# Performance work log

Hardware: AMD Instinct MI355X
Metric: run time of the kernel (lower is better)

The kernel has to match this reference:

```python
import jax, jax.numpy as jnp
import numpy as np

NEG = -1e32
EPS_LN = 1e-5

def _layer_norm(x, w, b):
    mu = jnp.mean(x, axis=-1, keepdims=True)
    var = jnp.mean((x - mu) ** 2, axis=-1, keepdims=True)
    return (x - mu) / jnp.sqrt(var + EPS_LN) * w + b

def setup_inputs() -> dict:
    key = jax.random.key(0)
    ks = jax.random.split(key, 10)
    B, S, D, H, F = 2, 2048, 1024, 16, 4096
    s = 0.02
    return {
        "query": jax.random.normal(ks[0], (B, S, D), jnp.float32),
        "key": jax.random.normal(ks[1], (B, S, D), jnp.float32),
        "values": jax.random.normal(ks[2], (B, S, D), jnp.float32),
        "Wk": jax.random.normal(ks[3], (D, D), jnp.float32) * s,
        "bk": jnp.zeros((D,), jnp.float32),
        "Wv": jax.random.normal(ks[4], (D, D), jnp.float32) * s,
        "bv": jnp.zeros((D,), jnp.float32),
        "Wo": jax.random.normal(ks[5], (D, D), jnp.float32) * s,
        "bo": jnp.zeros((D,), jnp.float32),
        "gammas": jax.random.normal(ks[6], (H, 1, 1), jnp.float32),
        "ln1_w": jnp.ones((D,), jnp.float32),
        "ln1_b": jnp.zeros((D,), jnp.float32),
        "W1": jax.random.normal(ks[7], (F, D), jnp.float32) * s,
        "b1": jnp.zeros((F,), jnp.float32),
        "W2": jax.random.normal(ks[8], (D, F), jnp.float32) * s,
        "b2": jnp.zeros((D,), jnp.float32),
        "ln2_w": jnp.ones((D,), jnp.float32),
        "ln2_b": jnp.zeros((D,), jnp.float32),
        "mask": 1,
    }

def _forward(query, key, values, Wk, bk, Wv, bv, Wo, bo, gammas,
             ln1_w, ln1_b, W1, b1, W2, b2, ln2_w, ln2_b, mask):
    B, S, D = query.shape
    H = gammas.shape[0]
    dk = D // H
    # kq_same=True: q and k both use k_linear
    def proj(x, W, b):
        return (x @ W.T + b).reshape(B, S, H, dk).transpose(0, 2, 1, 3)  # bhsd
    q = proj(query, Wk, bk)
    k = proj(key, Wk, bk)
    v = proj(values, Wv, bv)

    scores = jnp.einsum("bhqd,bhkd->bhqk", q, k) / np.sqrt(dk).astype(np.float32)
    # src_mask: np.triu(ones, k=mask)==0 -> allowed where j <= i + mask - 1
    allow = jnp.tril(jnp.ones((S, S), bool), k=mask - 1)[None, None]  # (1,1,S,S)

    # --- distance decay (no_grad block in torch) ---
    scores_ = jax.nn.softmax(jnp.where(allow, scores, NEG), axis=-1)
    scores_ = scores_ * allow.astype(scores_.dtype)
    distcum = jnp.cumsum(scores_, axis=-1)
    disttotal = jnp.sum(scores_, axis=-1, keepdims=True)
    idx = jnp.arange(S)
    position_effect = jnp.abs(idx[:, None] - idx[None, :]).astype(jnp.float32)[None, None]
    dist_scores = jnp.sqrt(jnp.clip((disttotal - distcum) * position_effect, 0.0, None))
    gamma = -jax.nn.softplus(gammas)[None]  # (1,H,1,1)
    total_effect = jnp.clip(jnp.exp(dist_scores * gamma), 1e-5, 1e5)
    total_effect = jax.lax.stop_gradient(total_effect)
    # ---

    scores = scores * total_effect
    scores = jnp.where(allow, scores, NEG)
    attn = jax.nn.softmax(scores, axis=-1)
    out = jnp.einsum("bhqk,bhkd->bhqd", attn, v)
    concat = out.transpose(0, 2, 1, 3).reshape(B, S, D)
    query2 = concat @ Wo.T + bo

    x = _layer_norm(query + query2, ln1_w, ln1_b)
    ff = jax.nn.relu(x @ W1.T + b1) @ W2.T + b2
    x = _layer_norm(x + ff, ln2_w, ln2_b)
    return x

def reference(query, key, values, Wk, bk, Wv, bv, Wo, bo, gammas,
              ln1_w, ln1_b, W1, b1, W2, b2, ln2_w, ln2_b, mask):
    return _forward(query, key, values, Wk, bk, Wv, bv, Wo, bo, gammas,
                    ln1_w, ln1_b, W1, b1, W2, b2, ln2_w, ln2_b, mask)
```

## Files before the change

### kernel.cpp

```cpp
#include <hip/hip_runtime.h>
#include <hip/hip_bf16.h>

#define B_   2
#define S_   2048
#define D_   1024
#define H_   16
#define DK_  64
#define F_   4096
#define M_   (B_*S_)
#define PD   72

typedef __attribute__((ext_vector_type(8))) short short8;
typedef __attribute__((ext_vector_type(4))) float f32x4;

__device__ __forceinline__ float bf2f(unsigned short s) { return __uint_as_float(((unsigned int)s) << 16); }
__device__ __forceinline__ unsigned short f2bf(float f) {
    unsigned int u = __float_as_uint(f);
    u += 0x7fffu + ((u >> 16) & 1u);
    return (unsigned short)(u >> 16);
}

__device__ __forceinline__ bool probe_f32(const unsigned int* p) {
    return *p == 0x3F800000u;
}
__device__ __forceinline__ float ld1e(const void* p, size_t idx, bool f32) {
    return f32 ? ((const float*)p)[idx] : bf2f(((const unsigned short*)p)[idx]);
}
__device__ __forceinline__ void st1e(void* p, size_t idx, bool f32, float v) {
    if (f32) ((float*)p)[idx] = v;
    else     ((unsigned short*)p)[idx] = f2bf(v);
}

__device__ __forceinline__ void async16(void* lds, const void* g) {
    __builtin_amdgcn_global_load_lds(
        (const __attribute__((address_space(1))) void*)g,
        (__attribute__((address_space(3))) void*)lds, 16, 0, 0);
}

__device__ __forceinline__ unsigned int cvt_pk_bf16(float a, float b) {
    unsigned int r;
    asm("v_cvt_pk_bf16_f32 %0, %1, %2" : "=v"(r) : "v"(a), "v"(b));
    return r;
}

template <bool IS_MAX>
__device__ __forceinline__ float block_reduce(float val, float* buf, int tid) {
    buf[tid] = val;
    __syncthreads();
    #pragma unroll
    for (int off = 128; off > 0; off >>= 1) {
        if (tid < off) {
            float o = buf[tid + off];
            buf[tid] = IS_MAX ? fmaxf(buf[tid], o) : (buf[tid] + o);
        }
        __syncthreads();
    }
    float r = buf[0];
    __syncthreads();
    return r;
}

__global__ __launch_bounds__(256) void cvt_all(
    const void* __restrict__ W1, const void* __restrict__ W2,
    const void* __restrict__ Wk, const void* __restrict__ Wv,
    const void* __restrict__ Wo,
    const void* __restrict__ Qi, const void* __restrict__ Ki,
    const void* __restrict__ Vi,
    unsigned short* __restrict__ W1b, unsigned short* __restrict__ W2b,
    unsigned short* __restrict__ Wkb, unsigned short* __restrict__ Wvb,
    unsigned short* __restrict__ Wob,
    unsigned short* __restrict__ qcb, unsigned short* __restrict__ kcb,
    unsigned short* __restrict__ vcb,
    const unsigned int* __restrict__ probe)
{
    const bool p32 = probe_f32(probe);
    const int blk = blockIdx.x;
    const void* src;
    unsigned short* dst;
    int off;
    if (blk < 2048)      { src = W1; dst = W1b; off = blk; }
    else if (blk < 4096) { src = W2; dst = W2b; off = blk - 2048; }
    else if (blk < 4608) { src = Wk; dst = Wkb; off = blk - 4096; }
    else if (blk < 5120) { src = Wv; dst = Wvb; off = blk - 4608; }
    else if (blk < 5632) { src = Wo; dst = Wob; off = blk - 5120; }
    else if (blk < 7680) { if (!p32) return; src = Qi; dst = qcb; off = blk - 5632; }
    else if (blk < 9728) { if (!p32) return; src = Ki; dst = kcb; off = blk - 7680; }
    else                 { if (!p32) return; src = Vi; dst = vcb; off = blk - 9728; }
    const int i8 = (off * 256 + threadIdx.x) * 8;
    if (p32) {
        const float4 a = *(const float4*)((const float*)src + i8);
        const float4 b = *(const float4*)((const float*)src + i8 + 4);
        short8 o;
        o[0] = (short)f2bf(a.x); o[1] = (short)f2bf(a.y);
        o[2] = (short)f2bf(a.z); o[3] = (short)f2bf(a.w);
        o[4] = (short)f2bf(b.x); o[5] = (short)f2bf(b.y);
        o[6] = (short)f2bf(b.z); o[7] = (short)f2bf(b.w);
        *(short8*)(dst + i8) = o;
    } else {
        *(uint4*)(dst + i8) = *(const uint4*)((const unsigned short*)src + i8);
    }
}

template <int RELU, int AEXT, int CEXT>
__device__ __forceinline__ void gemm_body(
    const void* __restrict__ A,
    const unsigned short* __restrict__ W,
    const void* __restrict__ bias,
    void* __restrict__ C,
    int M, int N, int K, bool p32, int bx, int by)
{
    __shared__ unsigned short As[2][128 * 32];
    __shared__ unsigned short Ws[2][128 * 32];

    const bool a32 = AEXT && p32;
    const bool c32 = CEXT && p32;

    const int tid = threadIdx.x;
    const int lane = tid & 63;
    const int w = tid >> 6;
    const int wr = w >> 1;
    const int wc = w & 1;
    const int col16 = lane & 15;
    const int quad = lane >> 4;

    const int m0 = by * 128;
    const int n0 = bx * 128;

    const int c0 = tid, c1 = 256 + tid;
    const int r0 = c0 >> 2, kc0 = (c0 & 3) * 8;
    const int r1 = c1 >> 2, kc1 = (c1 & 3) * 8;

    f32x4 acc[4][4];
    #pragma unroll
    for (int mt = 0; mt < 4; mt++)
        #pragma unroll
        for (int nt = 0; nt < 4; nt++)
            acc[mt][nt] = (f32x4){0.f, 0.f, 0.f, 0.f};

    auto stage = [&](int bb, int k0) {
        async16(&Ws[bb][c0 * 8], W + (size_t)(n0 + r0) * K + k0 + kc0);
        async16(&Ws[bb][c1 * 8], W + (size_t)(n0 + r1) * K + k0 + kc1);
        if (a32) {
            const float* a0 = (const float*)A + (size_t)(m0 + r0) * K + k0 + kc0;
            const float* a1 = (const float*)A + (size_t)(m0 + r1) * K + k0 + kc1;
            const float4 x0 = *(const float4*)a0, y0 = *(const float4*)(a0 + 4);
            const float4 x1 = *(const float4*)a1, y1 = *(const float4*)(a1 + 4);
            short8 s0, s1;
            s0[0] = (short)f2bf(x0.x); s0[1] = (short)f2bf(x0.y);
            s0[2] = (short)f2bf(x0.z); s0[3] = (short)f2bf(x0.w);
            s0[4] = (short)f2bf(y0.x); s0[5] = (short)f2bf(y0.y);
            s0[6] = (short)f2bf(y0.z); s0[7] = (short)f2bf(y0.w);
            s1[0] = (short)f2bf(x1.x); s1[1] = (short)f2bf(x1.y);
            s1[2] = (short)f2bf(x1.z); s1[3] = (short)f2bf(x1.w);
            s1[4] = (short)f2bf(y1.x); s1[5] = (short)f2bf(y1.y);
            s1[6] = (short)f2bf(y1.z); s1[7] = (short)f2bf(y1.w);
            *(short8*)&As[bb][c0 * 8] = s0;
            *(short8*)&As[bb][c1 * 8] = s1;
        } else {
            const unsigned short* Ab = (const unsigned short*)A;
            async16(&As[bb][c0 * 8], Ab + (size_t)(m0 + r0) * K + k0 + kc0);
            async16(&As[bb][c1 * 8], Ab + (size_t)(m0 + r1) * K + k0 + kc1);
        }
    };

    stage(0, 0);
    __syncthreads();
    int cur = 0;
    for (int k0 = 0; k0 < K; k0 += 32) {
        const int nxt = cur ^ 1;
        if (k0 + 32 < K) stage(nxt, k0 + 32);

        short8 av[4], bv[4];
        #pragma unroll
        for (int mt = 0; mt < 4; mt++)
            av[mt] = *(const short8*)&As[cur][(wr * 64 + mt * 16 + col16) * 32 + quad * 8];
        #pragma unroll
        for (int nt = 0; nt < 4; nt++)
            bv[nt] = *(const short8*)&Ws[cur][(wc * 64 + nt * 16 + col16) * 32 + quad * 8];
        #pragma unroll
        for (int mt = 0; mt < 4; mt++)
            #pragma unroll
            for (int nt = 0; nt < 4; nt++)
                acc[mt][nt] = __builtin_amdgcn_mfma_f32_16x16x32_bf16(
                    av[mt], bv[nt], acc[mt][nt], 0, 0, 0);
        __syncthreads();
        cur = nxt;
    }

    #pragma unroll
    for (int mt = 0; mt < 4; mt++) {
        const int row = m0 + wr * 64 + mt * 16 + quad * 4;
        #pragma unroll
        for (int nt = 0; nt < 4; nt++) {
            const int col = n0 + wc * 64 + nt * 16 + col16;
            const float bb = ld1e(bias, col, p32);
            #pragma unroll
            for (int r = 0; r < 4; r++) {
                float v = acc[mt][nt][r] + bb;
                if (RELU) v = fmaxf(v, 0.f);
                st1e(C, (size_t)(row + r) * N + col, c32, v);
            }
        }
    }
}

template <int RELU, int AEXT, int CEXT>
__global__ __launch_bounds__(256) void gemm_mf(
    const void* __restrict__ A,
    const unsigned short* __restrict__ W,
    const void* __restrict__ bias,
    void* __restrict__ C,
    int M, int N, int K,
    const unsigned int* __restrict__ probe)
{
    gemm_body<RELU, AEXT, CEXT>(A, W, bias, C, M, N, K, probe_f32(probe),
                                blockIdx.x, blockIdx.y);
}

__global__ __launch_bounds__(256) void gemm_proj(
    const void* __restrict__ q_orig, const void* __restrict__ k_orig,
    const void* __restrict__ v_orig,
    const unsigned short* __restrict__ qcb, const unsigned short* __restrict__ kcb,
    const unsigned short* __restrict__ vcb,
    const unsigned short* __restrict__ Wkb, const unsigned short* __restrict__ Wvb,
    const void* __restrict__ bk, const void* __restrict__ bv,
    unsigned short* __restrict__ qw, unsigned short* __restrict__ kw,
    unsigned short* __restrict__ vw,
    const unsigned int* __restrict__ probe)
{
    const bool p32 = probe_f32(probe);
    const int z = blockIdx.z;
    const unsigned short* W = (z == 2) ? Wvb : Wkb;
    const void* bias = (z == 2) ? bv : bk;
    void* C = (z == 0) ? (void*)qw : (z == 1) ? (void*)kw : (void*)vw;
    if (z == 2 && p32 && vcb == nullptr) {
        gemm_body<0, 1, 0>(v_orig, W, bias, C, M_, D_, D_, p32,
                           blockIdx.x, blockIdx.y);
    } else {
        const void* A = (z == 0) ? (p32 ? (const void*)qcb : q_orig)
                      : (z == 1) ? (p32 ? (const void*)kcb : k_orig)
                                 : (p32 ? (const void*)vcb : v_orig);
        gemm_body<0, 0, 0>(A, W, bias, C, M_, D_, D_, p32,
                           blockIdx.x, blockIdx.y);
    }
}

__global__ __launch_bounds__(256) void vtrans(
    const unsigned short* __restrict__ vw,
    unsigned short* __restrict__ vtg)
{
    __shared__ unsigned short T[64 * PD];
    const int tid = threadIdx.x;
    const int bid = blockIdx.x;
    const int bh = bid & 31;
    const int kt = bid >> 5;
    const int h = bh & 15, b = bh >> 4;
    #pragma unroll
    for (int cc = 0; cc < 2; cc++) {
        const int c = tid + cc * 256;
        const int key = c >> 3, dc = c & 7;
        const uint4 u = *(const uint4*)(vw + (size_t)(b * S_ + kt * 64 + key) * D_ + h * 64 + dc * 8);
        unsigned short* dst = &T[(dc * 8) * PD + key];
        dst[0 * PD] = (unsigned short)(u.x & 0xffff);
        dst[1 * PD] = (unsigned short)(u.x >> 16);
        dst[2 * PD] = (unsigned short)(u.y & 0xffff);
        dst[3 * PD] = (unsigned short)(u.y >> 16);
        dst[4 * PD] = (unsigned short)(u.z & 0xffff);
        dst[5 * PD] = (unsigned short)(u.z >> 16);
        dst[6 * PD] = (unsigned short)(u.w & 0xffff);
        dst[7 * PD] = (unsigned short)(u.w >> 16);
    }
    __syncthreads();
    #pragma unroll
    for (int cc = 0; cc < 2; cc++) {
        const int c = tid + cc * 256;
        const int d = c >> 3, kc = c & 7;
        const uint4 u = *(const uint4*)&T[d * PD + kc * 8];
        *(uint4*)(vtg + ((size_t)bh * 64 + d) * S_ + kt * 64 + kc * 8) = u;
    }
}

__global__ __launch_bounds__(256) void attn_mfma(
    const unsigned short* __restrict__ qw,
    const unsigned short* __restrict__ kw,
    const unsigned short* __restrict__ vtg,
    const void* __restrict__ gam,
    const int* __restrict__ maskp,
    unsigned short* __restrict__ outc,
    const unsigned int* __restrict__ probe)
{
    __shared__ unsigned short Qs[64 * PD];
    __shared__ unsigned short Ks[64 * PD];
    __shared__ unsigned short Vt[64 * PD];
    __shared__ float ctS[64 * 33];
    __shared__ float rT1S[64];
    unsigned int* const Pu = (unsigned int*)Qs;

    const bool p32 = probe_f32(probe);
    const int tid = threadIdx.x;
    const int lane = tid & 63;
    const int w = tid >> 6;
    const int col16 = lane & 15;
    const int quad = lane >> 4;
    const int bid = blockIdx.x;
    const int qt = 31 - (bid >> 5);
    const int bh = bid & 31;
    const int h = bh & 15;
    const int b = bh >> 4;
    const int i0 = qt * 64;

    const int mask = *maskp;
    long long nje = (long long)i0 + 63 + (long long)mask;
    int njmax = (nje > S_) ? S_ : (int)nje;
    if (njmax < 1) njmax = 1;
    const int ntiles = (njmax + 63) >> 6;
    long long fm = (long long)i0 + (long long)mask - 64;
    int nfull = 0;
    if (fm >= 0) {
        long long v = (fm >> 6) + 1;
        nfull = (v > ntiles) ? ntiles : (int)v;
    }

    const float L2E = 1.44269504088896f;
    const float gval = ld1e(gam, h, p32);
    const float sp = (gval > 20.f) ? gval : log1pf(__expf(gval));
    const float g2 = -sp * L2E;
    const float SC2 = 0.125f * L2E;

    const int myrow = i0 + w * 16 + col16;
    const int limq = myrow + mask - quad * 4;

    #pragma unroll
    for (int cc = 0; cc < 2; cc++) {
        const int c = tid + cc * 256;
        const int row = c >> 3, dc = c & 7;
        const uint4 u = *(const uint4*)(qw + (size_t)(b * S_ + i0 + row) * D_ + h * 64 + dc * 8);
        *(uint4*)&Qs[row * PD + dc * 8] = u;
    }
    __syncthreads();

    short8 avq[2];
    #pragma unroll
    for (int ks = 0; ks < 2; ks++)
        avq[ks] = *(const short8*)&Qs[(w * 16 + col16) * PD + ks * 32 + quad * 8];

    for (int t = 0; t < ntiles; t++) {
        const int j0 = t * 64;
        __syncthreads();
        #pragma unroll
        for (int cc = 0; cc < 2; cc++) {
            const int c = tid + cc * 256;
            const int row = c >> 3, dc = c & 7;
            const uint4 u = *(const uint4*)(kw + (size_t)(b * S_ + j0 + row) * D_ + h * 64 + dc * 8);
            *(uint4*)&Ks[row * PD + dc * 8] = u;
        }
        __syncthreads();

        f32x4 acc[4];
        #pragma unroll
        for (int nt = 0; nt < 4; nt++) acc[nt] = (f32x4){0.f, 0.f, 0.f, 0.f};
        #pragma unroll
        for (int ks = 0; ks < 2; ks++)
            #pragma unroll
            for (int nt = 0; nt < 4; nt++) {
                const short8 kv = *(const short8*)&Ks[(nt * 16 + col16) * PD + ks * 32 + quad * 8];
                acc[nt] = __builtin_amdgcn_mfma_f32_16x16x32_bf16(kv, avq[ks], acc[nt], 0, 0, 0);
            }

        if (t >= nfull) {
            #pragma unroll
            for (int nt = 0; nt < 4; nt++) {
                const int Ln = limq - j0 - nt * 16;
                #pragma unroll
                for (int r = 0; r < 4; r++)
                    acc[nt][r] = (r < Ln) ? acc[nt][r] : -3.0e38f;
            }
        }

        float cs = 0.f;
        #pragma unroll
        for (int nt = 0; nt < 4; nt++)
            #pragma unroll
            for (int r = 0; r < 4; r++)
                cs += __builtin_amdgcn_exp2f(acc[nt][r] * SC2);
        cs += __shfl_xor(cs, 16, 64);
        cs += __shfl_xor(cs, 32, 64);

        if (lane < 16)
            ctS[(w * 16 + lane) * 33 + t] = cs;
    }

    __syncthreads();
    if (lane < 16) {
        const int row = w * 16 + lane;
        float runv = 0.f;
        for (int t = 0; t < ntiles; t++) {
            const float e = ctS[row * 33 + t];
            ctS[row * 33 + t] = runv;
            runv += e;
        }
        rT1S[row] = 1.0f / runv;
    }
    __syncthreads();

    const float rT1 = rT1S[w * 16 + col16];

    float l2 = 0.f;
    f32x4 O[4];
    #pragma unroll
    for (int nt = 0; nt < 4; nt++) O[nt] = (f32x4){0.f, 0.f, 0.f, 0.f};

    for (int t = 0; t < ntiles; t++) {
        const int j0 = t * 64;
        __syncthreads();
        #pragma unroll
        for (int cc = 0; cc < 2; cc++) {
            const int c = tid + cc * 256;
            const int row = c >> 3, dc = c & 7;
            const uint4 u = *(const uint4*)(kw + (size_t)(b * S_ + j0 + row) * D_ + h * 64 + dc * 8);
            *(uint4*)&Ks[row * PD + dc * 8] = u;
        }
        #pragma unroll
        for (int cc = 0; cc < 2; cc++) {
            const int c = tid + cc * 256;
            const int d = c >> 3, kc = c & 7;
            const uint4 u = *(const uint4*)(vtg + ((size_t)bh * 64 + d) * S_ + j0 + kc * 8);
            *(uint4*)&Vt[d * PD + kc * 8] = u;
        }
        __syncthreads();

        f32x4 acc[4];
        #pragma unroll
        for (int nt = 0; nt < 4; nt++) acc[nt] = (f32x4){0.f, 0.f, 0.f, 0.f};
        #pragma unroll
        for (int ks = 0; ks < 2; ks++)
            #pragma unroll
            for (int nt = 0; nt < 4; nt++) {
                const short8 kv = *(const short8*)&Ks[(nt * 16 + col16) * PD + ks * 32 + quad * 8];
                acc[nt] = __builtin_amdgcn_mfma_f32_16x16x32_bf16(kv, avq[ks], acc[nt], 0, 0, 0);
            }

        if (t >= nfull) {
            #pragma unroll
            for (int nt = 0; nt < 4; nt++) {
                const int Ln = limq - j0 - nt * 16;
                #pragma unroll
                for (int r = 0; r < 4; r++)
                    acc[nt][r] = (r < Ln) ? acc[nt][r] : -3.0e38f;
            }
        }

        float s2v[4][4], loc[4][4], run4[4];
        #pragma unroll
        for (int nt = 0; nt < 4; nt++) {
            float rr = 0.f;
            #pragma unroll
            for (int r = 0; r < 4; r++) {
                const float s2 = acc[nt][r] * SC2;
                s2v[nt][r] = s2;
                rr += __builtin_amdgcn_exp2f(s2);
                loc[nt][r] = rr;
            }
            run4[nt] = rr;
        }
        float excl[4], tot[4];
        #pragma unroll
        for (int nt = 0; nt < 4; nt++) {
            float v = run4[nt];
            const float u1 = __shfl_up(v, 16, 64); if (quad >= 1) v += u1;
            const float u2 = __shfl_up(v, 32, 64); if (quad >= 2) v += u2;
            excl[nt] = v - run4[nt];
            tot[nt] = __shfl(v, col16 + 48, 64);
        }

        const float pref = ctS[(w * 16 + col16) * 33 + t];
        float Cb = pref;
        #pragma unroll
        for (int nt = 0; nt < 4; nt++) {
            const float CeR = (Cb + excl[nt]) * rT1;
            const float d0f = (float)(myrow - j0 - nt * 16 - quad * 4);
            float p4[4];
            #pragma unroll
            for (int r = 0; r < 4; r++) {
                const float cumn = __builtin_fmaf(loc[nt][r], rT1, CeR);
                const float rem = fmaxf(1.f - cumn, 0.f);
                const float pe = fabsf(d0f - (float)r);
                const float te = fmaxf(
                    __builtin_amdgcn_exp2f(g2 * __builtin_amdgcn_sqrtf(rem * pe)), 1e-5f);
                const float tv = s2v[nt][r] * te;
                p4[r] = __builtin_amdgcn_exp2f(tv);
                l2 += p4[r];
            }
            uint2 pk;
            pk.x = cvt_pk_bf16(p4[0], p4[1]);
            pk.y = cvt_pk_bf16(p4[2], p4[3]);
            *(uint2*)&Pu[(w * 16 + col16) * 36 + nt * 8 + quad * 2] = pk;
            Cb += tot[nt];
        }

        const short8 pa0 = *(const short8*)&Pu[(w * 16 + col16) * 36 + 0 * 16 + quad * 4];
        const short8 pa1 = *(const short8*)&Pu[(w * 16 + col16) * 36 + 1 * 16 + quad * 4];
        #pragma unroll
        for (int nt = 0; nt < 4; nt++) {
            const short8 bv0 = *(const short8*)&Vt[(nt * 16 + col16) * PD + 0 * 32 + quad * 8];
            const short8 bv1 = *(const short8*)&Vt[(nt * 16 + col16) * PD + 1 * 32 + quad * 8];
            O[nt] = __builtin_amdgcn_mfma_f32_16x16x32_bf16(pa0, bv0, O[nt], 0, 0, 0);
            O[nt] = __builtin_amdgcn_mfma_f32_16x16x32_bf16(pa1, bv1, O[nt], 0, 0, 0);
        }
    }

    l2 += __shfl_xor(l2, 16, 64);
    l2 += __shfl_xor(l2, 32, 64);
    const float rl2 = 1.0f / l2;
    float rl2O[4];
    #pragma unroll
    for (int r = 0; r < 4; r++) rl2O[r] = __shfl(rl2, quad * 4 + r, 64);
    #pragma unroll
    for (int nt = 0; nt < 4; nt++)
        #pragma unroll
        for (int r = 0; r < 4; r++)
            outc[(size_t)(b * S_ + i0 + w * 16 + quad * 4 + r) * D_ + h * 64 + nt * 16 + col16] =
                f2bf(O[nt][r] * rl2O[r]);
}

__global__ __launch_bounds__(256) void ln_fused(
    const void* __restrict__ A,
    const void* __restrict__ Bq,
    const void* __restrict__ w,
    const void* __restrict__ bias,
    void* __restrict__ out,
    const unsigned int* __restrict__ probe, int aext, int bext, int oext)
{
    __shared__ float xs[D_];
    __shared__ float red[256];
    const bool p32 = probe_f32(probe);
    const bool a32 = aext && p32;
    const bool b32 = bext && p32;
    const bool o32 = oext && p32;

    const int tid = threadIdx.x;
    const size_t row = (size_t)blockIdx.x * D_;

    float lsum = 0.f;
    #pragma unroll
    for (int qq = 0; qq < 4; qq++) {
        const int j = tid + qq * 256;
        const float x = ld1e(A, row + j, a32) + ld1e(Bq, row + j, b32);
        xs[j] = x;
        lsum += x;
    }
    const float mu = block_reduce<false>(lsum, red, tid) * (1.0f / D_);

    float lv = 0.f;
    #pragma unroll
    for (int qq = 0; qq < 4; qq++) {
        const int j = tid + qq * 256;
        const float dd = xs[j] - mu;
        lv += dd * dd;
    }
    const float var = block_reduce<false>(lv, red, tid) * (1.0f / D_);
    const float rs = rsqrtf(var + 1e-5f);

    #pragma unroll
    for (int qq = 0; qq < 4; qq++) {
        const int j = tid + qq * 256;
        const float o = (xs[j] - mu) * rs * ld1e(w, j, p32) + ld1e(bias, j, p32);
        st1e(out, row + j, o32, o);
    }
}

extern "C" void kernel_launch(void* const* d_in, const int* in_sizes, int n_in,
                              void* d_out, int out_size, void* d_ws, size_t ws_size,
                              hipStream_t stream)
{
    (void)in_sizes; (void)n_in; (void)out_size;

    const void* query  = d_in[0];
    const void* key_   = d_in[1];
    const void* values = d_in[2];
    const void* Wk     = d_in[3];
    const void* bk     = d_in[4];
    const void* Wv     = d_in[5];
    const void* bv     = d_in[6];
    const void* Wo     = d_in[7];
    const void* bo     = d_in[8];
    const void* gammas = d_in[9];
    const void* ln1w   = d_in[10];
    const void* ln1b   = d_in[11];
    const void* W1     = d_in[12];
    const void* b1     = d_in[13];
    const void* W2     = d_in[14];
    const void* b2     = d_in[15];
    const void* ln2w   = d_in[16];
    const void* ln2b   = d_in[17];
    const int*  maskp  = (const int*)d_in[18];
    const unsigned int* probe = (const unsigned int*)ln1w;

    char* ws = (char*)d_ws;
    const size_t MiB = 1024 * 1024;
    unsigned short* W1b = (unsigned short*)(ws + 0 * MiB);
    unsigned short* W2b = (unsigned short*)(ws + 8 * MiB);
    unsigned short* Wkb = (unsigned short*)(ws + 16 * MiB);
    unsigned short* Wvb = (unsigned short*)(ws + 18 * MiB);
    unsigned short* Wob = (unsigned short*)(ws + 20 * MiB);
    unsigned short* qw  = (unsigned short*)(ws + 22 * MiB);
    unsigned short* kw  = (unsigned short*)(ws + 30 * MiB);
    unsigned short* vw  = (unsigned short*)(ws + 38 * MiB);
    unsigned short* cw  = (unsigned short*)(ws + 46 * MiB);
    unsigned short* vtg = (unsigned short*)(ws + 54 * MiB);
    unsigned short* x1  = (unsigned short*)(ws + 22 * MiB);
    unsigned short* fh  = (unsigned short*)(ws + 30 * MiB);
    unsigned short* qc  = (unsigned short*)(ws + 46 * MiB);
    unsigned short* kc  = (unsigned short*)(ws + 54 * MiB);
    unsigned short* vc  = (ws_size >= (size_t)70 * MiB)
                          ? (unsigned short*)(ws + 62 * MiB) : nullptr;

    const dim3 blk(256);
    const int cvtgrid = vc ? 11776 : 9728;
    cvt_all<<<dim3(cvtgrid), blk, 0, stream>>>(
        W1, W2, Wk, Wv, Wo, query, key_, values,
        W1b, W2b, Wkb, Wvb, Wob, qc, kc, vc, probe);
    gemm_proj<<<dim3(D_ / 128, M_ / 128, 3), blk, 0, stream>>>(
        query, key_, values, qc, kc, vc, Wkb, Wvb, bk, bv, qw, kw, vw, probe);
    vtrans<<<dim3(1024), blk, 0, stream>>>(vw, vtg);
    attn_mfma<<<dim3(B_ * H_ * (S_ / 64)), blk, 0, stream>>>(
        qw, kw, vtg, gammas, maskp, cw, probe);
    gemm_mf<0, 0, 0><<<dim3(D_ / 128, M_ / 128), blk, 0, stream>>>(
        cw, Wob, bo, x1, M_, D_, D_, probe);
    ln_fused<<<dim3(M_), blk, 0, stream>>>(query, x1, ln1w, ln1b, x1, probe, 1, 0, 0);
    gemm_mf<1, 0, 0><<<dim3(F_ / 128, M_ / 128), blk, 0, stream>>>(
        x1, W1b, b1, fh, M_, F_, D_, probe);
    gemm_mf<0, 0, 1><<<dim3(D_ / 128, M_ / 128), blk, 0, stream>>>(
        fh, W2b, b2, d_out, M_, D_, F_, probe);
    ln_fused<<<dim3(M_), blk, 0, stream>>>(x1, d_out, ln2w, ln2b, d_out, probe, 0, 1, 1);
}
```

Measured before the change: 478.4 us.

## Split K across two thread groups in N=1024 GEMMs with LDS reduction

Adds a 512-thread GEMM kernel in which two 256-thread groups each take half of the K dimension for the same 128x128 tile. The partial sums are combined through shared memory before bias and store. It replaces the Wo projection and the W2 down-projection, whose grids of 256 tiles give few waves per CU on this GPU. The cost is more shared memory per block, an extra reduction pass, and possibly lower occupancy.

```diff
diff --git a/kernel.cpp b/kernel.cpp
--- a/kernel.cpp
+++ b/kernel.cpp
@@ -217,6 +217,114 @@
                                 blockIdx.x, blockIdx.y);
 }
 
+template <int RELU, int CEXT>
+__global__ __launch_bounds__(512) void gemm_sk(
+    const unsigned short* __restrict__ A,
+    const unsigned short* __restrict__ W,
+    const void* __restrict__ bias,
+    void* __restrict__ C,
+    int M, int N, int K,
+    const unsigned int* __restrict__ probe)
+{
+    __shared__ unsigned short SS[2][2][2][128 * 32];
+    float* const R = (float*)&SS[0][0][0][0];
+
+    const bool p32 = probe_f32(probe);
+    const bool c32 = CEXT && p32;
+
+    const int tid = threadIdx.x;
+    const int g = tid >> 8;
+    const int tl = tid & 255;
+    const int lane = tl & 63;
+    const int w = tl >> 6;
+    const int wr = w >> 1;
+    const int wc = w & 1;
+    const int col16 = lane & 15;
+    const int quad = lane >> 4;
+
+    const int m0 = blockIdx.y * 128;
+    const int n0 = blockIdx.x * 128;
+
+    const int c0 = tl, c1 = 256 + tl;
+    const int r0 = c0 >> 2, kc0 = (c0 & 3) * 8;
+    const int r1 = c1 >> 2, kc1 = (c1 & 3) * 8;
+
+    const int Kh = K >> 1;
+    const int kbeg = g * Kh;
+
+    f32x4 acc[4][4];
+    #pragma unroll
+    for (int mt = 0; mt < 4; mt++)
+        #pragma unroll
+        for (int nt = 0; nt < 4; nt++)
+            acc[mt][nt] = (f32x4){0.f, 0.f, 0.f, 0.f};
+
+    auto stage = [&](int bb, int k0) {
+        async16(&SS[g][bb][1][c0 * 8], W + (size_t)(n0 + r0) * K + k0 + kc0);
+        async16(&SS[g][bb][1][c1 * 8], W + (size_t)(n0 + r1) * K + k0 + kc1);
+        async16(&SS[g][bb][0][c0 * 8], A + (size_t)(m0 + r0) * K + k0 + kc0);
+        async16(&SS[g][bb][0][c1 * 8], A + (size_t)(m0 + r1) * K + k0 + kc1);
+    };
+
+    stage(0, kbeg);
+    __syncthreads();
+    int cur = 0;
+    for (int kk = 0; kk < Kh; kk += 32) {
+        const int nxt = cur ^ 1;
+        if (kk + 32 < Kh) stage(nxt, kbeg + kk + 32);
+
+        short8 av[4], bv[4];
+        #pragma unroll
+        for (int mt = 0; mt < 4; mt++)
+            av[mt] = *(const short8*)&SS[g][cur][0][(wr * 64 + mt * 16 + col16) * 32 + quad * 8];
+        #pragma unroll
+        for (int nt = 0; nt < 4; nt++)
+            bv[nt] = *(const short8*)&SS[g][cur][1][(wc * 64 + nt * 16 + col16) * 32 + quad * 8];
+        #pragma unroll
+        for (int mt = 0; mt < 4; mt++)
+            #pragma unroll
+            for (int nt = 0; nt < 4; nt++)
+                acc[mt][nt] = __builtin_amdgcn_mfma_f32_16x16x32_bf16(
+                    av[mt], bv[nt], acc[mt][nt], 0, 0, 0);
+        __syncthreads();
+        cur = nxt;
+    }
+
+    __syncthreads();
+    if (g == 1) {
+        #pragma unroll
+        for (int mt = 0; mt < 4; mt++)
+            #pragma unroll
+            for (int nt = 0; nt < 4; nt++) {
+                const int lrow = wr * 64 + mt * 16 + quad * 4;
+                const int lcol = wc * 64 + nt * 16 + col16;
+                #pragma unroll
+                for (int r = 0; r < 4; r++)
+                    R[(lrow + r) * 128 + lcol] = acc[mt][nt][r];
+            }
+    }
+    __syncthreads();
+    if (g == 0) {
+        #pragma unroll
+        for (int mt = 0; mt < 4; mt++) {
+            const int lrow = wr * 64 + mt * 16 + quad * 4;
+            const int row = m0 + lrow;
+            #pragma unroll
+            for (int nt = 0; nt < 4; nt++) {
+                const int lcol = wc * 64 + nt * 16 + col16;
+                const int col = n0 + lcol;
+                const float bb = ld1e(bias, col, p32);
+                #pragma unroll
+                for (int r = 0; r < 4; r++) {
+                    float v = acc[mt][nt][r] + R[(lrow + r) * 128 + lcol] + bb;
+                    if (RELU) v = fmaxf(v, 0.f);
+                    st1e(C, (size_t)(row + r) * N + col, c32, v);
+                }
+            }
+        }
+    }
+}
+
 __global__ __launch_bounds__(256) void gemm_proj(
     const void* __restrict__ q_orig, const void* __restrict__ k_orig,
     const void* __restrict__ v_orig,
@@ -616,6 +724,7 @@
                           ? (unsigned short*)(ws + 62 * MiB) : nullptr;
 
     const dim3 blk(256);
+    const dim3 blk5(512);
     const int cvtgrid = vc ? 11776 : 9728;
     cvt_all<<<dim3(cvtgrid), blk, 0, stream>>>(
         W1, W2, Wk, Wv, Wo, query, key_, values,
@@ -625,12 +734,12 @@
     vtrans<<<dim3(1024), blk, 0, stream>>>(vw, vtg);
     attn_mfma<<<dim3(B_ * H_ * (S_ / 64)), blk, 0, stream>>>(
         qw, kw, vtg, gammas, maskp, cw, probe);
-    gemm_mf<0, 0, 0><<<dim3(D_ / 128, M_ / 128), blk, 0, stream>>>(
+    gemm_sk<0, 0><<<dim3(D_ / 128, M_ / 128), blk5, 0, stream>>>(
         cw, Wob, bo, x1, M_, D_, D_, probe);
     ln_fused<<<dim3(M_), blk, 0, stream>>>(query, x1, ln1w, ln1b, x1, probe, 1, 0, 0);
     gemm_mf<1, 0, 0><<<dim3(F_ / 128, M_ / 128), blk, 0, stream>>>(
         x1, W1b, b1, fh, M_, F_, D_, probe);
-    gemm_mf<0, 0, 1><<<dim3(D_ / 128, M_ / 128), blk, 0, stream>>>(
+    gemm_sk<0, 1><<<dim3(D_ / 128, M_ / 128), blk5, 0, stream>>>(
         fh, W2b, b2, d_out, M_, D_, F_, probe);
     ln_fused<<<dim3(M_), blk, 0, stream>>>(x1, d_out, ln2w, ln2b, d_out, probe, 0, 1, 1);
 }
```

Result: faster. 453.0 us (-5.3%).

## Deepen GEMM LDS pipeline with swizzle and drop attention prefix-sum shared pass

Applied to the files above, without the earlier changes.

The GEMM main loop moves from a double buffer to a 3- or 4-stage LDS ring. It uses explicit vmcnt waits and raw barriers in place of __syncthreads, so more global loads stay in flight per iteration. The LDS tile layout is XOR-swizzled across the k-chunks to reduce bank conflicts on the fragment reads. In the attention kernel, the per-tile column sums no longer go to shared memory followed by a separate prefix scan: the row total comes from a register reduction and the running prefix is carried across tiles. The deeper buffers raise LDS use per block, which may lower occupancy, and the hand-counted vmcnt values must match the real number of outstanding loads.

```diff
diff --git a/kernel.cpp b/kernel.cpp
--- a/kernel.cpp
+++ b/kernel.cpp
@@ -101,7 +101,7 @@
     }
 }
 
-template <int RELU, int AEXT, int CEXT>
+template <int RELU, int AEXT, int CEXT, int NBUF>
 __device__ __forceinline__ void gemm_body(
     const void* __restrict__ A,
     const unsigned short* __restrict__ W,
@@ -109,8 +109,8 @@
     void* __restrict__ C,
     int M, int N, int K, bool p32, int bx, int by)
 {
-    __shared__ unsigned short As[2][128 * 32];
-    __shared__ unsigned short Ws[2][128 * 32];
+    __shared__ unsigned short As[NBUF][128 * 32];
+    __shared__ unsigned short Ws[NBUF][128 * 32];
 
     const bool a32 = AEXT && p32;
     const bool c32 = CEXT && p32;
@@ -127,8 +127,10 @@
     const int n0 = bx * 128;
 
     const int c0 = tid, c1 = 256 + tid;
-    const int r0 = c0 >> 2, kc0 = (c0 & 3) * 8;
-    const int r1 = c1 >> 2, kc1 = (c1 & 3) * 8;
+    const int r0 = c0 >> 2, kc0 = (((c0 & 3) ^ ((c0 >> 3) & 3)) * 8);
+    const int r1 = c1 >> 2, kc1 = (((c1 & 3) ^ ((c1 >> 3) & 3)) * 8);
+
+    const int fcol = ((quad ^ ((col16 >> 1) & 3)) * 8);
 
     f32x4 acc[4][4];
     #pragma unroll
@@ -163,28 +165,49 @@
         }
     };
 
-    stage(0, 0);
-    __syncthreads();
+    #pragma unroll
+    for (int pb = 0; pb <= NBUF - 2; pb++) stage(pb, pb * 32);
+    if (a32) {
+        asm volatile("s_waitcnt vmcnt(0) lgkmcnt(0)" ::: "memory");
+    } else if constexpr (NBUF == 3) {
+        asm volatile("s_waitcnt vmcnt(4)" ::: "memory");
+    } else {
+        asm volatile("s_waitcnt vmcnt(8)" ::: "memory");
+    }
+    __builtin_amdgcn_s_barrier();
+
     int cur = 0;
     for (int k0 = 0; k0 < K; k0 += 32) {
-        const int nxt = cur ^ 1;
-        if (k0 + 32 < K) stage(nxt, k0 + 32);
+        const int pf = k0 + (NBUF - 1) * 32;
+        int nb = cur + (NBUF - 1); if (nb >= NBUF) nb -= NBUF;
+        if (pf < K) stage(nb, pf);
 
         short8 av[4], bv[4];
         #pragma unroll
         for (int mt = 0; mt < 4; mt++)
-            av[mt] = *(const short8*)&As[cur][(wr * 64 + mt * 16 + col16) * 32 + quad * 8];
+            av[mt] = *(const short8*)&As[cur][(wr * 64 + mt * 16 + col16) * 32 + fcol];
         #pragma unroll
         for (int nt = 0; nt < 4; nt++)
-            bv[nt] = *(const short8*)&Ws[cur][(wc * 64 + nt * 16 + col16) * 32 + quad * 8];
+            bv[nt] = *(const short8*)&Ws[cur][(wc * 64 + nt * 16 + col16) * 32 + fcol];
         #pragma unroll
         for (int mt = 0; mt < 4; mt++)
             #pragma unroll
             for (int nt = 0; nt < 4; nt++)
                 acc[mt][nt] = __builtin_amdgcn_mfma_f32_16x16x32_bf16(
                     av[mt], bv[nt], acc[mt][nt], 0, 0, 0);
-        __syncthreads();
-        cur = nxt;
+
+        if (a32) {
+            asm volatile("s_waitcnt vmcnt(0) lgkmcnt(0)" ::: "memory");
+        } else if constexpr (NBUF == 3) {
+            if (k0 + 64 < K) asm volatile("s_waitcnt vmcnt(4)" ::: "memory");
+            else             asm volatile("s_waitcnt vmcnt(0)" ::: "memory");
+        } else {
+            if (k0 + 96 < K)      asm volatile("s_waitcnt vmcnt(8)" ::: "memory");
+            else if (k0 + 64 < K) asm volatile("s_waitcnt vmcnt(4)" ::: "memory");
+            else                  asm volatile("s_waitcnt vmcnt(0)" ::: "memory");
+        }
+        __builtin_amdgcn_s_barrier();
+        cur = cur + 1; if (cur >= NBUF) cur = 0;
     }
 
     #pragma unroll
@@ -204,7 +227,7 @@
     }
 }
 
-template <int RELU, int AEXT, int CEXT>
+template <int RELU, int AEXT, int CEXT, int NBUF>
 __global__ __launch_bounds__(256) void gemm_mf(
     const void* __restrict__ A,
     const unsigned short* __restrict__ W,
@@ -213,8 +236,8 @@
     int M, int N, int K,
     const unsigned int* __restrict__ probe)
 {
-    gemm_body<RELU, AEXT, CEXT>(A, W, bias, C, M, N, K, probe_f32(probe),
-                                blockIdx.x, blockIdx.y);
+    gemm_body<RELU, AEXT, CEXT, NBUF>(A, W, bias, C, M, N, K, probe_f32(probe),
+                                      blockIdx.x, blockIdx.y);
 }
 
 __global__ __launch_bounds__(256) void gemm_proj(
@@ -234,14 +257,14 @@
     const void* bias = (z == 2) ? bv : bk;
     void* C = (z == 0) ? (void*)qw : (z == 1) ? (void*)kw : (void*)vw;
     if (z == 2 && p32 && vcb == nullptr) {
-        gemm_body<0, 1, 0>(v_orig, W, bias, C, M_, D_, D_, p32,
-                           blockIdx.x, blockIdx.y);
+        gemm_body<0, 1, 0, 3>(v_orig, W, bias, C, M_, D_, D_, p32,
+                              blockIdx.x, blockIdx.y);
     } else {
         const void* A = (z == 0) ? (p32 ? (const void*)qcb : q_orig)
                       : (z == 1) ? (p32 ? (const void*)kcb : k_orig)
                                  : (p32 ? (const void*)vcb : v_orig);
-        gemm_body<0, 0, 0>(A, W, bias, C, M_, D_, D_, p32,
-                           blockIdx.x, blockIdx.y);
+        gemm_body<0, 0, 0, 3>(A, W, bias, C, M_, D_, D_, p32,
+                              blockIdx.x, blockIdx.y);
     }
 }
 
@@ -292,8 +315,6 @@
     __shared__ unsigned short Qs[64 * PD];
     __shared__ unsigned short Ks[64 * PD];
     __shared__ unsigned short Vt[64 * PD];
-    __shared__ float ctS[64 * 33];
-    __shared__ float rT1S[64];
     unsigned int* const Pu = (unsigned int*)Qs;
 
     const bool p32 = probe_f32(probe);
@@ -344,6 +365,7 @@
     for (int ks = 0; ks < 2; ks++)
         avq[ks] = *(const short8*)&Qs[(w * 16 + col16) * PD + ks * 32 + quad * 8];
 
+    float T1l = 0.f;
     for (int t = 0; t < ntiles; t++) {
         const int j0 = t * 64;
         __syncthreads();
@@ -377,35 +399,18 @@
             }
         }
 
-        float cs = 0.f;
         #pragma unroll
         for (int nt = 0; nt < 4; nt++)
             #pragma unroll
             for (int r = 0; r < 4; r++)
-                cs += __builtin_amdgcn_exp2f(acc[nt][r] * SC2);
-        cs += __shfl_xor(cs, 16, 64);
-        cs += __shfl_xor(cs, 32, 64);
-
-        if (lane < 16)
-            ctS[(w * 16 + lane) * 33 + t] = cs;
-    }
-
-    __syncthreads();
-    if (lane < 16) {
-        const int row = w * 16 + lane;
-        float runv = 0.f;
-        for (int t = 0; t < ntiles; t++) {
-            const float e = ctS[row * 33 + t];
-            ctS[row * 33 + t] = runv;
-            runv += e;
-        }
-        rT1S[row] = 1.0f / runv;
-    }
-    __syncthreads();
-
-    const float rT1 = rT1S[w * 16 + col16];
+                T1l += __builtin_amdgcn_exp2f(acc[nt][r] * SC2);
+    }
+    T1l += __shfl_xor(T1l, 16, 64);
+    T1l += __shfl_xor(T1l, 32, 64);
+    const float rT1 = 1.0f / T1l;
 
     float l2 = 0.f;
+    float Cb_run = 0.f;
     f32x4 O[4];
     #pragma unroll
     for (int nt = 0; nt < 4; nt++) O[nt] = (f32x4){0.f, 0.f, 0.f, 0.f};
@@ -473,8 +478,7 @@
             tot[nt] = __shfl(v, col16 + 48, 64);
         }
 
-        const float pref = ctS[(w * 16 + col16) * 33 + t];
-        float Cb = pref;
+        float Cb = Cb_run;
         #pragma unroll
         for (int nt = 0; nt < 4; nt++) {
             const float CeR = (Cb + excl[nt]) * rT1;
@@ -497,6 +501,7 @@
             *(uint2*)&Pu[(w * 16 + col16) * 36 + nt * 8 + quad * 2] = pk;
             Cb += tot[nt];
         }
+        Cb_run = Cb;
 
         const short8 pa0 = *(const short8*)&Pu[(w * 16 + col16) * 36 + 0 * 16 + quad * 4];
         const short8 pa1 = *(const short8*)&Pu[(w * 16 + col16) * 36 + 1 * 16 + quad * 4];
@@ -625,12 +630,12 @@
     vtrans<<<dim3(1024), blk, 0, stream>>>(vw, vtg);
     attn_mfma<<<dim3(B_ * H_ * (S_ / 64)), blk, 0, stream>>>(
         qw, kw, vtg, gammas, maskp, cw, probe);
-    gemm_mf<0, 0, 0><<<dim3(D_ / 128, M_ / 128), blk, 0, stream>>>(
+    gemm_mf<0, 0, 0, 4><<<dim3(D_ / 128, M_ / 128), blk, 0, stream>>>(
         cw, Wob, bo, x1, M_, D_, D_, probe);
     ln_fused<<<dim3(M_), blk, 0, stream>>>(query, x1, ln1w, ln1b, x1, probe, 1, 0, 0);
-    gemm_mf<1, 0, 0><<<dim3(F_ / 128, M_ / 128), blk, 0, stream>>>(
+    gemm_mf<1, 0, 0, 3><<<dim3(F_ / 128, M_ / 128), blk, 0, stream>>>(
         x1, W1b, b1, fh, M_, F_, D_, probe);
-    gemm_mf<0, 0, 1><<<dim3(D_ / 128, M_ / 128), blk, 0, stream>>>(
+    gemm_mf<0, 0, 1, 4><<<dim3(D_ / 128, M_ / 128), blk, 0, stream>>>(
         fh, W2b, b2, d_out, M_, D_, F_, probe);
     ln_fused<<<dim3(M_), blk, 0, stream>>>(x1, d_out, ln2w, ln2b, d_out, probe, 0, 1, 1);
 }
```

Result: slower. 510.1 us (+6.6%).
